# Optimization experiments

Measured on AMD Instinct MI355X. Metric: run time of the kernel, lower is better.

## Reference

```python
import jax, jax.numpy as jnp
import numpy as np

D_MODEL = 1024
N_HEADS = 16
D_K = D_MODEL // N_HEADS
BATCH = 8
SEQ = 1024
ROPE_BASE = 10000.0


def setup_inputs() -> dict:
    key = jax.random.key(0)
    ks = jax.random.split(key, 9)
    s = 1.0 / np.sqrt(D_MODEL)
    return {
        "x": jax.random.normal(ks[0], (BATCH, SEQ, D_MODEL), dtype=jnp.float32),
        "position_ids": jnp.arange(SEQ, dtype=jnp.int32)[None, :],
        "Wq": jax.random.normal(ks[1], (D_MODEL, D_MODEL), dtype=jnp.float32) * s,
        "bq": jnp.zeros((D_MODEL,), dtype=jnp.float32),
        "Wk": jax.random.normal(ks[2], (D_MODEL, D_MODEL), dtype=jnp.float32) * s,
        "bk": jnp.zeros((D_MODEL,), dtype=jnp.float32),
        "Wv": jax.random.normal(ks[3], (D_MODEL, D_MODEL), dtype=jnp.float32) * s,
        "bv": jnp.zeros((D_MODEL,), dtype=jnp.float32),
        "Wo": jax.random.normal(ks[4], (D_MODEL, D_MODEL), dtype=jnp.float32) * s,
        "bo": jnp.zeros((D_MODEL,), dtype=jnp.float32),
    }


def _apply_rope(t, position_ids):
    # t: [B, H, S, D_K]; position_ids: [1, S] (broadcast over batch)
    half = D_K // 2
    inv_freq = 1.0 / (ROPE_BASE ** (jnp.arange(half, dtype=jnp.float32) * 2.0 / D_K))
    ang = position_ids.astype(jnp.float32)[..., None] * inv_freq  # [1, S, half]
    cos = jnp.cos(ang)[:, None, :, :]  # [1, 1, S, half]
    sin = jnp.sin(ang)[:, None, :, :]
    t1, t2 = jnp.split(t, 2, axis=-1)
    return jnp.concatenate([t1 * cos - t2 * sin, t1 * sin + t2 * cos], axis=-1)


def reference(x, position_ids, Wq, bq, Wk, bk, Wv, bv, Wo, bo):
    B, S, D = x.shape
    def proj(W, b):
        # torch Linear: x @ W.T + b
        y = jnp.einsum('bsd,ed->bse', x, W) + b
        return y.reshape(B, S, N_HEADS, D_K).transpose(0, 2, 1, 3)  # [B,H,S,Dk]
    Q = proj(Wq, bq)
    K = proj(Wk, bk)
    V = proj(Wv, bv)
    Q = _apply_rope(Q, position_ids)
    K = _apply_rope(K, position_ids)
    scores = jnp.einsum('bhqd,bhkd->bhqk', Q, K) / jnp.sqrt(jnp.float32(D_K))
    attn = jax.nn.softmax(scores, axis=-1)
    out = jnp.einsum('bhqk,bhkd->bhqd', attn, V)
    out = out.transpose(0, 2, 1, 3).reshape(B, S, D)
    return jnp.einsum('bsd,ed->bse', out, Wo) + bo
```

## Files before the change

kernel.cpp:

```cpp
#include <hip/hip_runtime.h>
#include <hip/hip_bf16.h>


typedef __bf16 bf16_t;
typedef __bf16 bf16x8 __attribute__((ext_vector_type(8)));
typedef float  f32x4  __attribute__((ext_vector_type(4)));

static __device__ __forceinline__ f32x4 mfma16(bf16x8 a, bf16x8 b, f32x4 c) {
  return __builtin_amdgcn_mfma_f32_16x16x32_bf16(a, b, c, 0, 0, 0);
}

#if __has_builtin(__builtin_amdgcn_exp2f)
#define EXP2F(x) __builtin_amdgcn_exp2f(x)
#else
#define EXP2F(x) exp2f(x)
#endif

__global__ void k_prep(const float* __restrict__ x, const float* __restrict__ Wq,
                       const float* __restrict__ Wk, const float* __restrict__ Wv,
                       const float* __restrict__ Wo, const int* __restrict__ pos,
                       bf16_t* __restrict__ Xf, bf16_t* __restrict__ Wf,
                       float2* __restrict__ rt) {
  const int bid = blockIdx.x;
  const int t = threadIdx.x;
  if (bid < 4096) {
    int g = bid * 256 + t;
    int rg = g >> 11, kt = (g >> 6) & 31, lane = g & 63;
    int m = rg * 16 + (lane & 15);
    int k = kt * 32 + (lane >> 4) * 8;
    const float* s = x + (size_t)m * 1024 + k;
    float4 v0 = *(const float4*)s;
    float4 v1 = *(const float4*)(s + 4);
    union { bf16_t b[8]; } pk;
    pk.b[0] = (bf16_t)v0.x; pk.b[1] = (bf16_t)v0.y; pk.b[2] = (bf16_t)v0.z; pk.b[3] = (bf16_t)v0.w;
    pk.b[4] = (bf16_t)v1.x; pk.b[5] = (bf16_t)v1.y; pk.b[6] = (bf16_t)v1.z; pk.b[7] = (bf16_t)v1.w;
    __builtin_memcpy(Xf + (size_t)g * 8, pk.b, 16);
  } else if (bid < 6144) {
    int g = (bid - 4096) * 256 + t;
    int rg = g >> 11, kt = (g >> 6) & 31, lane = g & 63;
    const float* src = (rg < 64) ? Wq : (rg < 128) ? Wk : (rg < 192) ? Wv : Wo;
    int row = (rg & 63) * 16 + (lane & 15);
    int k = kt * 32 + (lane >> 4) * 8;
    const float* s = src + (size_t)row * 1024 + k;
    float4 v0 = *(const float4*)s;
    float4 v1 = *(const float4*)(s + 4);
    union { bf16_t b[8]; } pk;
    pk.b[0] = (bf16_t)v0.x; pk.b[1] = (bf16_t)v0.y; pk.b[2] = (bf16_t)v0.z; pk.b[3] = (bf16_t)v0.w;
    pk.b[4] = (bf16_t)v1.x; pk.b[5] = (bf16_t)v1.y; pk.b[6] = (bf16_t)v1.z; pk.b[7] = (bf16_t)v1.w;
    __builtin_memcpy(Wf + (size_t)g * 8, pk.b, 16);
  } else {
    int rb = bid - 6144;
    int s = rb * 8 + (t >> 5);
    int f = t & 31;
    float p = (float)pos[s];
    float inv = powf(10000.0f, -(float)(2 * f) / 64.0f);
    float a = p * inv;
    rt[s * 32 + f] = make_float2(cosf(a), sinf(a));
  }
}

#define GEMM_DIRECT_BODY(AfBase, BfBase)                                       \
  const int t = threadIdx.x;                                                   \
  const int lane = t & 63, w = t >> 6;                                         \
  const int hi = lane >> 4, c = lane & 15;                                     \
  const int wm = w >> 2, wn = w & 3;                                           \
  const bf16_t* Ab = (AfBase) + (size_t)((i0 >> 4) + wm * 4) * 16384 + lane * 8; \
  const bf16_t* Bb = (BfBase) + (size_t)((e0 >> 4) + wn * 4) * 16384 + lane * 8; \
  bf16x8 pa0, pa1, pa2, pa3, pb0, pb1, pb2, pb3;                               \
  bf16x8 qa0, qa1, qa2, qa3, qb0, qb1, qb2, qb3;                               \
  f32x4 acc[4][4] = {};                                                        \
  auto loadP = [&](int kt) {                                                   \
    pa0 = *(const bf16x8*)(Ab + kt * 512);                                     \
    pa1 = *(const bf16x8*)(Ab + 16384 + kt * 512);                             \
    pa2 = *(const bf16x8*)(Ab + 32768 + kt * 512);                             \
    pa3 = *(const bf16x8*)(Ab + 49152 + kt * 512);                             \
    pb0 = *(const bf16x8*)(Bb + kt * 512);                                     \
    pb1 = *(const bf16x8*)(Bb + 16384 + kt * 512);                             \
    pb2 = *(const bf16x8*)(Bb + 32768 + kt * 512);                             \
    pb3 = *(const bf16x8*)(Bb + 49152 + kt * 512);                             \
  };                                                                           \
  auto loadQ = [&](int kt) {                                                   \
    qa0 = *(const bf16x8*)(Ab + kt * 512);                                     \
    qa1 = *(const bf16x8*)(Ab + 16384 + kt * 512);                             \
    qa2 = *(const bf16x8*)(Ab + 32768 + kt * 512);                             \
    qa3 = *(const bf16x8*)(Ab + 49152 + kt * 512);                             \
    qb0 = *(const bf16x8*)(Bb + kt * 512);                                     \
    qb1 = *(const bf16x8*)(Bb + 16384 + kt * 512);                             \
    qb2 = *(const bf16x8*)(Bb + 32768 + kt * 512);                             \
    qb3 = *(const bf16x8*)(Bb + 49152 + kt * 512);                             \
  };                                                                           \
  auto compP = [&]() {                                                         \
    bf16x8 a_[4] = {pa0, pa1, pa2, pa3}, b_[4] = {pb0, pb1, pb2, pb3};         \
    __builtin_amdgcn_s_setprio(1);                                             \
    _Pragma("unroll") for (int fr = 0; fr < 4; ++fr)                           \
      _Pragma("unroll") for (int nc = 0; nc < 4; ++nc)                         \
        acc[fr][nc] = mfma16(a_[fr], b_[nc], acc[fr][nc]);                     \
    __builtin_amdgcn_s_setprio(0);                                             \
  };                                                                           \
  auto compQ = [&]() {                                                         \
    bf16x8 a_[4] = {qa0, qa1, qa2, qa3}, b_[4] = {qb0, qb1, qb2, qb3};         \
    __builtin_amdgcn_s_setprio(1);                                             \
    _Pragma("unroll") for (int fr = 0; fr < 4; ++fr)                           \
      _Pragma("unroll") for (int nc = 0; nc < 4; ++nc)                         \
        acc[fr][nc] = mfma16(a_[fr], b_[nc], acc[fr][nc]);                     \
    __builtin_amdgcn_s_setprio(0);                                             \
  };                                                                           \
  loadP(0);                                                                    \
  loadQ(1);                                                                    \
  _Pragma("unroll 3")                                                          \
  for (int jj = 0; jj < 15; ++jj) {                                            \
    compP(); loadP(jj * 2 + 2);                                                \
    compQ(); loadQ(jj * 2 + 3);                                                \
  }                                                                            \
  compP();                                                                     \
  compQ();

__global__ __launch_bounds__(512) void k_gemm_qkv(
    const bf16_t* __restrict__ Xf, const bf16_t* __restrict__ Wf,
    const float* __restrict__ bq, const float* __restrict__ bk,
    const float* __restrict__ bv, const float2* __restrict__ rt,
    bf16_t* __restrict__ Qh, bf16_t* __restrict__ Kg, bf16_t* __restrict__ Vg) {
  const int bid = blockIdx.x;
  const int x = bid & 7, q = bid >> 3;
  const int i0 = (x * 8 + (q & 7)) * 128;
  const int e0 = (q >> 3) * 256;

  GEMM_DIRECT_BODY(Xf, Wf)

  const int z = e0 >> 10;
  const int ez0 = (e0 & 1023) + wn * 64;
  const int h = ez0 >> 6;
  const float* bias = (z == 0) ? bq : (z == 1) ? bk : bv;
  if (z == 2) {
#pragma unroll
    for (int fr = 0; fr < 4; ++fr) {
      int i = i0 + wm * 64 + fr * 16 + hi * 4;
      int b_ = i >> 10, sbase = i & 1023;
      int bhv = b_ * 16 + h;
      int lane_ = c | (((sbase >> 3) & 3) << 4);
#pragma unroll
      for (int nc = 0; nc < 4; ++nc) {
        float bv_ = bias[ez0 + nc * 16 + c];
        union { bf16_t b[4]; } pk;
#pragma unroll
        for (int r = 0; r < 4; ++r) pk.b[r] = (bf16_t)(acc[fr][nc][r] + bv_);
        size_t g = (size_t)(bhv * 4 + nc) * 32 + (sbase >> 5);
        __builtin_memcpy(&Vg[g * 512 + lane_ * 8 + (sbase & 7)], pk.b, 8);
      }
    }
  } else if (z == 0) {
    const float scl = 0.18033688011112042f;
#pragma unroll
    for (int fr = 0; fr < 4; ++fr) {
      int i = i0 + wm * 64 + fr * 16 + hi * 4;
      int b_ = i >> 10, sbase = i & 1023;
      size_t obase = (size_t)((b_ * 16 + h) * 1024);
#pragma unroll
      for (int nc = 0; nc < 2; ++nc) {
        int f = nc * 16 + c;
        float b1_ = bias[ez0 + f], b2_ = bias[ez0 + f + 32];
#pragma unroll
        for (int r = 0; r < 4; ++r) {
          int s = sbase + r;
          float2 cs = rt[s * 32 + f];
          float q1 = acc[fr][nc][r] + b1_;
          float q2 = acc[fr][nc + 2][r] + b2_;
          Qh[(obase + s) * 64 + f] = (bf16_t)((q1 * cs.x - q2 * cs.y) * scl);
          Qh[(obase + s) * 64 + f + 32] = (bf16_t)((q1 * cs.y + q2 * cs.x) * scl);
        }
      }
    }
  } else {
#pragma unroll
    for (int fr = 0; fr < 4; ++fr) {
      int i = i0 + wm * 64 + fr * 16 + hi * 4;
      int b_ = i >> 10, sbase = i & 1023;
      bf16_t* gb = Kg + (size_t)((b_ * 16 + h) * 64 + (sbase >> 4)) * 1024;
#pragma unroll
      for (int nc = 0; nc < 2; ++nc) {
        int f = nc * 16 + c;
        float b1_ = bias[ez0 + f], b2_ = bias[ez0 + f + 32];
        int laneHi = (nc * 2 + (c >> 3)) << 4;
#pragma unroll
        for (int r = 0; r < 4; ++r) {
          int s = sbase + r;
          float2 cs = rt[s * 32 + f];
          float q1 = acc[fr][nc][r] + b1_;
          float q2 = acc[fr][nc + 2][r] + b2_;
          size_t off = (size_t)((hi * 4 + r) | laneHi) * 8 + (c & 7);
          gb[off] = (bf16_t)(q1 * cs.x - q2 * cs.y);
          gb[off + 512] = (bf16_t)(q1 * cs.y + q2 * cs.x);
        }
      }
    }
  }
}

__global__ __launch_bounds__(512) void k_gemm_out(
    const bf16_t* __restrict__ Ogf, const bf16_t* __restrict__ Wf,
    const float* __restrict__ bo, float* __restrict__ out) {
  const int bid = blockIdx.x;
  const int x = bid & 7, q = bid >> 3;
  const int i0 = (x * 8 + (q & 7)) * 128;
  const int e0 = (q >> 3) * 256;
  const bf16_t* WfO = Wf + (size_t)192 * 16384;

  GEMM_DIRECT_BODY(Ogf, WfO)

#pragma unroll
  for (int fr = 0; fr < 4; ++fr) {
    int i = i0 + wm * 64 + fr * 16 + hi * 4;
#pragma unroll
    for (int nc = 0; nc < 4; ++nc) {
      int e = e0 + wn * 64 + nc * 16 + c;
      float bv_ = bo[e];
#pragma unroll
      for (int r = 0; r < 4; ++r)
        out[(size_t)(i + r) * 1024 + e] = acc[fr][nc][r] + bv_;
    }
  }
}

__global__ __launch_bounds__(512) void k_attn(
    const bf16_t* __restrict__ Qh, const bf16_t* __restrict__ Kg,
    const bf16_t* __restrict__ Vg, bf16_t* __restrict__ Ogf) {
  __shared__ alignas(16) char PL[8][2048];
  const int t = threadIdx.x;
  const int lane = t & 63, w = t >> 6;
  const int hi = lane >> 4, c = lane & 15;
  const int bid = blockIdx.x;
  const int wg = (bid & 7) * 32 + (bid >> 3);
  const int bh = wg >> 1, half = wg & 1;
  const int q0 = half * 512 + w * 64;
  const size_t qbase = (size_t)bh * 64 * 1024;

  const bf16_t* Kb = Kg + (size_t)bh * 65536 + lane * 8;
  const bf16_t* Vb = Vg + (size_t)bh * 65536 + lane * 8;

  bf16x8 qf[4][2];
#pragma unroll
  for (int ss = 0; ss < 4; ++ss)
#pragma unroll
    for (int kk = 0; kk < 2; ++kk)
      qf[ss][kk] = *(const bf16x8*)&Qh[qbase + (size_t)(q0 + ss * 16 + c) * 64 +
                                       kk * 32 + hi * 8];

  f32x4 o[4][4] = {};
  float m_[4] = {-1e30f, -1e30f, -1e30f, -1e30f};
  float l_[4] = {0.f, 0.f, 0.f, 0.f};
  char* const plw = &PL[w][0];

  bf16x8 kp[8], kq[8], vv[8];
#pragma unroll
  for (int i = 0; i < 8; ++i) kp[i] = *(const bf16x8*)(Kb + i * 512);

#define SM_PV(ST, M, L, O)                                                     \
  {                                                                            \
    float pmax = -1e30f;                                                       \
    _Pragma("unroll") for (int ni = 0; ni < 4; ++ni)                           \
      _Pragma("unroll") for (int r = 0; r < 4; ++r)                            \
        pmax = fmaxf(pmax, ST[ni][r]);                                         \
    pmax = fmaxf(pmax, __shfl_xor(pmax, 16));                                  \
    pmax = fmaxf(pmax, __shfl_xor(pmax, 32));                                  \
    float mn = fmaxf(M, pmax);                                                 \
    float scale = EXP2F(M - mn);                                               \
    M = mn;                                                                    \
    float psum = 0.f;                                                          \
    _Pragma("unroll") for (int ni = 0; ni < 4; ++ni) {                         \
      union { bf16_t b[4]; } pk;                                               \
      _Pragma("unroll") for (int r = 0; r < 4; ++r) {                          \
        float p = EXP2F(ST[ni][r] - mn);                                       \
        psum += p;                                                             \
        pk.b[r] = (bf16_t)p;                                                   \
      }                                                                        \
      __builtin_memcpy(plw + (ni * 2 + (hi >> 1)) * 256 + c * 16 + (hi & 1) * 8, \
                       pk.b, 8);                                               \
    }                                                                          \
    psum += __shfl_xor(psum, 16);                                              \
    psum += __shfl_xor(psum, 32);                                              \
    L = L * scale + psum;                                                      \
    _Pragma("unroll") for (int od = 0; od < 4; ++od)                           \
      _Pragma("unroll") for (int r = 0; r < 4; ++r) O[od][r] *= scale;         \
    bf16x8 pa[2];                                                              \
    __builtin_memcpy(&pa[0], plw + lane * 16, 16);                             \
    __builtin_memcpy(&pa[1], plw + 1024 + lane * 16, 16);                      \
    _Pragma("unroll") for (int od = 0; od < 4; ++od)                           \
      _Pragma("unroll") for (int kk = 0; kk < 2; ++kk)                         \
        O[od] = mfma16(vv[od * 2 + kk], pa[kk], O[od]);                        \
  }

#define ATTN_TILE(KS, KN, KT)                                                  \
  {                                                                            \
    _Pragma("unroll") for (int i = 0; i < 8; ++i)                              \
      vv[i] = *(const bf16x8*)(Vb + ((i >> 1) * 32 + (KT) * 2 + (i & 1)) * 512); \
    _Pragma("unroll") for (int ss = 0; ss < 4; ++ss) {                         \
      f32x4 st[4] = {};                                                        \
      _Pragma("unroll") for (int ni = 0; ni < 4; ++ni)                         \
        _Pragma("unroll") for (int kk = 0; kk < 2; ++kk)                       \
          st[ni] = mfma16(KS[ni * 2 + kk], qf[ss][kk], st[ni]);                \
      if (ss == 0 && (KT) + 1 < 16) {                                          \
        _Pragma("unroll") for (int i = 0; i < 8; ++i)                          \
          KN[i] = *(const bf16x8*)(Kb + (((KT) + 1) * 8 + i) * 512);           \
      }                                                                        \
      SM_PV(st, m_[ss], l_[ss], o[ss])                                         \
    }                                                                          \
  }

  for (int jj = 0; jj < 8; ++jj) {
    ATTN_TILE(kp, kq, jj * 2);
    ATTN_TILE(kq, kp, jj * 2 + 1);
  }
#undef ATTN_TILE
#undef SM_PV

  int b_ = bh >> 4, h = bh & 15;
  int rg0 = ((b_ << 10) + q0) >> 4;
#pragma unroll
  for (int ss = 0; ss < 4; ++ss) {
    float iv = 1.f / l_[ss];
#pragma unroll
    for (int od = 0; od < 4; ++od) {
      union { bf16_t b[4]; } pk;
#pragma unroll
      for (int r = 0; r < 4; ++r) pk.b[r] = (bf16_t)(o[ss][od][r] * iv);
      int kt2 = (h << 1) + (od >> 1);
      int lp = ((od & 1) * 2 + (hi >> 1)) * 16 + c;
      int el = (hi & 1) * 4;
      __builtin_memcpy(&Ogf[((size_t)((rg0 + ss) * 32 + kt2) * 64 + lp) * 8 + el],
                       pk.b, 8);
    }
  }
}

extern "C" void kernel_launch(void* const* d_in, const int* in_sizes, int n_in,
                              void* d_out, int out_size, void* d_ws, size_t ws_size,
                              hipStream_t stream) {
  const float* x = (const float*)d_in[0];
  const int* pos = (const int*)d_in[1];
  const float* Wq = (const float*)d_in[2];
  const float* bq = (const float*)d_in[3];
  const float* Wk = (const float*)d_in[4];
  const float* bk = (const float*)d_in[5];
  const float* Wv = (const float*)d_in[6];
  const float* bv = (const float*)d_in[7];
  const float* Wo = (const float*)d_in[8];
  const float* bo = (const float*)d_in[9];
  float* out = (float*)d_out;

  char* ws = (char*)d_ws;
  bf16_t* Xf = (bf16_t*)ws;
  bf16_t* Wf = (bf16_t*)(ws + (16u << 20));
  bf16_t* Vg = (bf16_t*)(ws + (24u << 20));
  float2* rt = (float2*)(ws + (42u << 20));
  bf16_t* Qh = (bf16_t*)d_out;
  bf16_t* Kg = (bf16_t*)d_out + (size_t)8 * 1024 * 1024;
  bf16_t* Ogf = Xf;

  k_prep<<<6272, 256, 0, stream>>>(x, Wq, Wk, Wv, Wo, pos, Xf, Wf, rt);
  k_gemm_qkv<<<768, 512, 0, stream>>>(Xf, Wf, bq, bk, bv, rt, Qh, Kg, Vg);
  k_attn<<<256, 512, 0, stream>>>(Qh, Kg, Vg, Ogf);
  k_gemm_out<<<256, 512, 0, stream>>>(Ogf, Wf, bo, out);
}
```

Before: 152.9 us.

## Deepen GEMM register prefetch to triple buffering and remap blocks per XCD

The direct-from-global GEMM body now keeps three register buffers (P/Q/R) in flight instead of two, so each k-tile load is issued two compute steps ahead to hide more global memory latency. The block-to-tile mapping for both the QKV and output GEMMs is also changed so that blocks sharing the same XCD (bid&7) cover a compact row/column region, improving L2 reuse of A and B tiles. The extra buffer adds eight bf16x8 registers per thread, which may raise register pressure and lower occupancy at 512 threads.

New measurement: 159.6 us. 4.4% more time.

```diff
diff --git a/kernel.cpp b/kernel.cpp
--- a/kernel.cpp
+++ b/kernel.cpp
@@ -68,6 +68,7 @@
   const bf16_t* Bb = (BfBase) + (size_t)((e0 >> 4) + wn * 4) * 16384 + lane * 8; \
   bf16x8 pa0, pa1, pa2, pa3, pb0, pb1, pb2, pb3;                               \
   bf16x8 qa0, qa1, qa2, qa3, qb0, qb1, qb2, qb3;                               \
+  bf16x8 ra0, ra1, ra2, ra3, rb0, rb1, rb2, rb3;                               \
   f32x4 acc[4][4] = {};                                                        \
   auto loadP = [&](int kt) {                                                   \
     pa0 = *(const bf16x8*)(Ab + kt * 512);                                     \
@@ -89,6 +90,16 @@
     qb2 = *(const bf16x8*)(Bb + 32768 + kt * 512);                             \
     qb3 = *(const bf16x8*)(Bb + 49152 + kt * 512);                             \
   };                                                                           \
+  auto loadR = [&](int kt) {                                                   \
+    ra0 = *(const bf16x8*)(Ab + kt * 512);                                     \
+    ra1 = *(const bf16x8*)(Ab + 16384 + kt * 512);                             \
+    ra2 = *(const bf16x8*)(Ab + 32768 + kt * 512);                             \
+    ra3 = *(const bf16x8*)(Ab + 49152 + kt * 512);                             \
+    rb0 = *(const bf16x8*)(Bb + kt * 512);                                     \
+    rb1 = *(const bf16x8*)(Bb + 16384 + kt * 512);                             \
+    rb2 = *(const bf16x8*)(Bb + 32768 + kt * 512);                             \
+    rb3 = *(const bf16x8*)(Bb + 49152 + kt * 512);                             \
+  };                                                                           \
   auto compP = [&]() {                                                         \
     bf16x8 a_[4] = {pa0, pa1, pa2, pa3}, b_[4] = {pb0, pb1, pb2, pb3};         \
     __builtin_amdgcn_s_setprio(1);                                             \
@@ -105,13 +116,24 @@
         acc[fr][nc] = mfma16(a_[fr], b_[nc], acc[fr][nc]);                     \
     __builtin_amdgcn_s_setprio(0);                                             \
   };                                                                           \
-  loadP(0);                                                                    \
-  loadQ(1);                                                                    \
+  auto compR = [&]() {                                                         \
+    bf16x8 a_[4] = {ra0, ra1, ra2, ra3}, b_[4] = {rb0, rb1, rb2, rb3};         \
+    __builtin_amdgcn_s_setprio(1);                                             \
+    _Pragma("unroll") for (int fr = 0; fr < 4; ++fr)                           \
+      _Pragma("unroll") for (int nc = 0; nc < 4; ++nc)                         \
+        acc[fr][nc] = mfma16(a_[fr], b_[nc], acc[fr][nc]);                     \
+    __builtin_amdgcn_s_setprio(0);                                             \
+  };                                                                           \
+  loadP(0); loadQ(1); loadR(2);                                                \
   _Pragma("unroll 3")                                                          \
-  for (int jj = 0; jj < 15; ++jj) {                                            \
-    compP(); loadP(jj * 2 + 2);                                                \
-    compQ(); loadQ(jj * 2 + 3);                                                \
+  for (int jj = 0; jj < 9; ++jj) {                                             \
+    compP(); loadP(jj * 3 + 3);                                                \
+    compQ(); loadQ(jj * 3 + 4);                                                \
+    compR(); loadR(jj * 3 + 5);                                                \
   }                                                                            \
+  compP(); loadP(30);                                                          \
+  compQ(); loadQ(31);                                                          \
+  compR();                                                                     \
   compP();                                                                     \
   compQ();
 
@@ -122,8 +144,8 @@
     bf16_t* __restrict__ Qh, bf16_t* __restrict__ Kg, bf16_t* __restrict__ Vg) {
   const int bid = blockIdx.x;
   const int x = bid & 7, q = bid >> 3;
-  const int i0 = (x * 8 + (q & 7)) * 128;
-  const int e0 = (q >> 3) * 256;
+  const int i0 = ((x >> 2) * 32 + q / 3) * 128;
+  const int e0 = ((x & 3) * 3 + q % 3) * 256;
 
   GEMM_DIRECT_BODY(Xf, Wf)
 
@@ -201,8 +223,8 @@
     const float* __restrict__ bo, float* __restrict__ out) {
   const int bid = blockIdx.x;
   const int x = bid & 7, q = bid >> 3;
-  const int i0 = (x * 8 + (q & 7)) * 128;
-  const int e0 = (q >> 3) * 256;
+  const int i0 = ((x >> 2) * 32 + q) * 128;
+  const int e0 = (x & 3) * 256;
   const bf16_t* WfO = Wf + (size_t)192 * 16384;
 
   GEMM_DIRECT_BODY(Ogf, WfO)
```
